# Optimization experiments

Measured on AMD Instinct MI355X. Metric: run time of the kernel, lower is better.

Reference implementation:

```python
import jax, jax.numpy as jnp
import numpy as np
from jax import lax

T = 32768
INPUT = 1024
HIDDEN = 1024
OUTPUT = 1024


def setup_inputs() -> dict:
    key = jax.random.key(0)
    k1, k2, k3, k4, k5 = jax.random.split(key, 5)
    return {
        "x": jax.random.normal(k1, (1, T, INPUT), dtype=jnp.float32),
        "W_i2h": jax.random.normal(k2, (HIDDEN, INPUT + HIDDEN), dtype=jnp.float32) * 0.02,
        "b_i2h": jax.random.normal(k3, (HIDDEN,), dtype=jnp.float32) * 0.02,
        "W_h2o": jax.random.normal(k4, (OUTPUT, HIDDEN), dtype=jnp.float32) * 0.02,
        "b_h2o": jax.random.normal(k5, (OUTPUT,), dtype=jnp.float32) * 0.02,
    }


def reference(x, W_i2h, b_i2h, W_h2o, b_h2o):
    # x: [1, T, input]; original iterates timesteps of x[0] with batch-1 state.
    seq = x[0]  # [T, input]
    h0 = jnp.zeros((1, HIDDEN), dtype=x.dtype)

    # Split i2h weight so we avoid a per-step concat: [hidden, input+hidden]
    W_x = W_i2h[:, :INPUT]   # acts on token
    W_h = W_i2h[:, INPUT:]   # acts on hidden

    def step(h, x_t):
        # h: [1, hidden], x_t: [input]
        h_new = jnp.tanh(x_t[None, :] @ W_x.T + h @ W_h.T + b_i2h)
        return h_new, None

    h_T, _ = lax.scan(step, h0, seq)
    # Original computes h2o every step but returns only the last output.
    output = h_T @ W_h2o.T + b_h2o  # [1, output]
    return output
```

## Files before the change

### kernel.cpp

```cpp
#include <hip/hip_runtime.h>

#define T_STEPS 32768
#define HID 1024
#define NWG 128
#define RPW 8
#define MBS 8
#define PRE_BYTES ((size_t)T_STEPS * HID * 2)
#define HP_BYTES  (2 * HID * MBS * 8)

typedef float vf4 __attribute__((ext_vector_type(4)));
typedef unsigned long long u64;

__device__ __forceinline__ unsigned short f2bf(float f) {
    unsigned u = __float_as_uint(f);
    u = (u + 0x7fffu + ((u >> 16) & 1u)) >> 16;
    return (unsigned short)u;
}
__device__ __forceinline__ float bf2f(unsigned short s) {
    return __uint_as_float(((unsigned)s) << 16);
}

#define BM 64
#define BN 64
#define BK 16
#define LDST 68

__global__ void __launch_bounds__(256) pre_gemm(
    const float* __restrict__ x, const float* __restrict__ Wi,
    const float* __restrict__ b, unsigned short* __restrict__ pre)
{
    __shared__ float As[BK * LDST];
    __shared__ float Bs[BK * LDST];
    const int tid = threadIdx.x;
    const int t0 = blockIdx.x * BM;
    const int j0 = blockIdx.y * BN;
    const int row = tid >> 2;
    const int kq  = tid & 3;
    const int tx  = tid & 15;
    const int ty  = tid >> 4;

    float c[4][4];
#pragma unroll
    for (int i = 0; i < 4; ++i)
#pragma unroll
        for (int j = 0; j < 4; ++j) c[i][j] = 0.f;

    for (int k0 = 0; k0 < 1024; k0 += BK) {
        float4 a4 = *(const float4*)&x[(size_t)(t0 + row) * 1024 + k0 + 4 * kq];
        float4 b4 = *(const float4*)&Wi[(size_t)(j0 + row) * 2048 + k0 + 4 * kq];
        __syncthreads();
        As[(4 * kq + 0) * LDST + row] = a4.x;
        As[(4 * kq + 1) * LDST + row] = a4.y;
        As[(4 * kq + 2) * LDST + row] = a4.z;
        As[(4 * kq + 3) * LDST + row] = a4.w;
        Bs[(4 * kq + 0) * LDST + row] = b4.x;
        Bs[(4 * kq + 1) * LDST + row] = b4.y;
        Bs[(4 * kq + 2) * LDST + row] = b4.z;
        Bs[(4 * kq + 3) * LDST + row] = b4.w;
        __syncthreads();
#pragma unroll
        for (int kk = 0; kk < BK; ++kk) {
            float4 av = *(const float4*)&As[kk * LDST + 4 * ty];
            float4 bv = *(const float4*)&Bs[kk * LDST + 4 * tx];
            c[0][0] = fmaf(av.x, bv.x, c[0][0]); c[0][1] = fmaf(av.x, bv.y, c[0][1]);
            c[0][2] = fmaf(av.x, bv.z, c[0][2]); c[0][3] = fmaf(av.x, bv.w, c[0][3]);
            c[1][0] = fmaf(av.y, bv.x, c[1][0]); c[1][1] = fmaf(av.y, bv.y, c[1][1]);
            c[1][2] = fmaf(av.y, bv.z, c[1][2]); c[1][3] = fmaf(av.y, bv.w, c[1][3]);
            c[2][0] = fmaf(av.z, bv.x, c[2][0]); c[2][1] = fmaf(av.z, bv.y, c[2][1]);
            c[2][2] = fmaf(av.z, bv.z, c[2][2]); c[2][3] = fmaf(av.z, bv.w, c[2][3]);
            c[3][0] = fmaf(av.w, bv.x, c[3][0]); c[3][1] = fmaf(av.w, bv.y, c[3][1]);
            c[3][2] = fmaf(av.w, bv.z, c[3][2]); c[3][3] = fmaf(av.w, bv.w, c[3][3]);
        }
    }

    float4 bias = *(const float4*)&b[j0 + 4 * tx];
#pragma unroll
    for (int i = 0; i < 4; ++i) {
        int r = t0 + 4 * ty + i;
        ushort4 u;
        u.x = f2bf(c[i][0] + bias.x);
        u.y = f2bf(c[i][1] + bias.y);
        u.z = f2bf(c[i][2] + bias.z);
        u.w = f2bf(c[i][3] + bias.w);
        *(ushort4*)&pre[(size_t)r * 1024 + j0 + 4 * tx] = u;
    }
}

__device__ __forceinline__ vf4 ldg4_pin(const float* p) {
    vf4 r;
    asm volatile("global_load_dwordx4 %0, %1, off\n\ts_waitcnt vmcnt(0)"
                 : "=v"(r) : "v"(p) : "memory");
    return r;
}
__device__ __forceinline__ u64 pack_hv(float v, unsigned t) {
    return ((u64)t << 32) | (u64)__float_as_uint(v);
}
__device__ __forceinline__ float fast_tanh(float x) {
    float a = fabsf(x);
    float e = __expf(a + a);
    float r = 1.f - 2.f * __builtin_amdgcn_rcpf(e + 1.f);
    return copysignf(r, x);
}

__global__ void __launch_bounds__(512, 2) rnn_rec(
    const unsigned short* __restrict__ pre,
    const float* __restrict__ Wi,
    const float* __restrict__ Wo,
    const float* __restrict__ bo,
    float* __restrict__ out,
    u64* hp)
{
    const int tid = threadIdx.x;
    const int w   = tid >> 6;
    const int l   = tid & 63;
    const int r   = blockIdx.x * RPW + w;

    __shared__ __align__(16) float hl[2][HID];
    __shared__ int s_abort;
    if (tid == 0) s_abort = 0;

    vf4 wv0, wv1, wv2, wv3;
    {
        const float* wp = Wi + (size_t)r * 2048 + 1024 + 4 * l;
        wv0 = ldg4_pin(wp + 0);
        wv1 = ldg4_pin(wp + 256);
        wv2 = ldg4_pin(wp + 512);
        wv3 = ldg4_pin(wp + 768);
    }
    __syncthreads();

    int budget = 8000000;
    const int e0 = 2 * tid, e1 = 2 * tid + 1;

    for (int t = 1; t <= T_STEPS; ++t) {
        const int par = (t - 1) & 1;

        float prev = 0.f;
        if (l == 0) prev = bf2f(pre[(size_t)(t - 1) * HID + r]);

        {
            const u64* s0 = hp + (size_t)par * (HID * MBS) + (size_t)e0 * MBS;
            const u64* s1 = hp + (size_t)par * (HID * MBS) + (size_t)e1 * MBS;
            const unsigned tg = (unsigned)(t - 1);
            u64 q0, q1;
            for (;;) {
                q0 = __hip_atomic_load(s0, __ATOMIC_RELAXED, __HIP_MEMORY_SCOPE_AGENT);
                q1 = __hip_atomic_load(s1, __ATOMIC_RELAXED, __HIP_MEMORY_SCOPE_AGENT);
                if (((unsigned)(q0 >> 32) == tg) & ((unsigned)(q1 >> 32) == tg)) break;
                if (--budget < 0) { s_abort = 1; break; }
            }
            float2 v;
            v.x = __uint_as_float((unsigned)q0);
            v.y = __uint_as_float((unsigned)q1);
            *(float2*)&hl[par][e0] = v;
        }
        __syncthreads();
        if (s_abort) return;

        const float* hb = hl[par];
        vf4 a0 = *(const vf4*)&hb[4 * l + 0];
        vf4 a1 = *(const vf4*)&hb[4 * l + 256];
        vf4 a2 = *(const vf4*)&hb[4 * l + 512];
        vf4 a3 = *(const vf4*)&hb[4 * l + 768];
        float acc0 = 0.f, acc1 = 0.f;
        acc0 = fmaf(wv0.x, a0.x, acc0); acc0 = fmaf(wv0.y, a0.y, acc0);
        acc0 = fmaf(wv0.z, a0.z, acc0); acc0 = fmaf(wv0.w, a0.w, acc0);
        acc1 = fmaf(wv1.x, a1.x, acc1); acc1 = fmaf(wv1.y, a1.y, acc1);
        acc1 = fmaf(wv1.z, a1.z, acc1); acc1 = fmaf(wv1.w, a1.w, acc1);
        acc0 = fmaf(wv2.x, a2.x, acc0); acc0 = fmaf(wv2.y, a2.y, acc0);
        acc0 = fmaf(wv2.z, a2.z, acc0); acc0 = fmaf(wv2.w, a2.w, acc0);
        acc1 = fmaf(wv3.x, a3.x, acc1); acc1 = fmaf(wv3.y, a3.y, acc1);
        acc1 = fmaf(wv3.z, a3.z, acc1); acc1 = fmaf(wv3.w, a3.w, acc1);
        float s = acc0 + acc1;
        s += __shfl_xor(s, 1);
        s += __shfl_xor(s, 2);
        s += __shfl_xor(s, 4);
        s += __shfl_xor(s, 8);
        s += __shfl_xor(s, 16);
        s += __shfl_xor(s, 32);

        if (l == 0) {
            float h = fast_tanh(prev + s);
            __hip_atomic_store(&hp[(size_t)(t & 1) * (HID * MBS) + (size_t)r * MBS],
                               pack_hv(h, (unsigned)t),
                               __ATOMIC_RELAXED, __HIP_MEMORY_SCOPE_AGENT);
        }
    }

    {
        const int par = T_STEPS & 1;
        const u64* s0 = hp + (size_t)par * (HID * MBS) + (size_t)e0 * MBS;
        const u64* s1 = hp + (size_t)par * (HID * MBS) + (size_t)e1 * MBS;
        const unsigned tg = (unsigned)T_STEPS;
        u64 q0, q1;
        for (;;) {
            q0 = __hip_atomic_load(s0, __ATOMIC_RELAXED, __HIP_MEMORY_SCOPE_AGENT);
            q1 = __hip_atomic_load(s1, __ATOMIC_RELAXED, __HIP_MEMORY_SCOPE_AGENT);
            if (((unsigned)(q0 >> 32) == tg) & ((unsigned)(q1 >> 32) == tg)) break;
            if (--budget < 0) { s_abort = 1; break; }
        }
        float2 v;
        v.x = __uint_as_float((unsigned)q0);
        v.y = __uint_as_float((unsigned)q1);
        *(float2*)&hl[0][e0] = v;
        __syncthreads();
        if (s_abort) return;

        const float* hb = hl[0];
        const float* wo = Wo + (size_t)r * 1024 + 4 * l;
        vf4 a0 = *(const vf4*)&hb[4 * l + 0];
        vf4 a1 = *(const vf4*)&hb[4 * l + 256];
        vf4 a2 = *(const vf4*)&hb[4 * l + 512];
        vf4 a3 = *(const vf4*)&hb[4 * l + 768];
        vf4 w0 = *(const vf4*)&wo[0];
        vf4 w1 = *(const vf4*)&wo[256];
        vf4 w2 = *(const vf4*)&wo[512];
        vf4 w3 = *(const vf4*)&wo[768];
        float acc0 = 0.f, acc1 = 0.f;
        acc0 = fmaf(w0.x, a0.x, acc0); acc0 = fmaf(w0.y, a0.y, acc0);
        acc0 = fmaf(w0.z, a0.z, acc0); acc0 = fmaf(w0.w, a0.w, acc0);
        acc1 = fmaf(w1.x, a1.x, acc1); acc1 = fmaf(w1.y, a1.y, acc1);
        acc1 = fmaf(w1.z, a1.z, acc1); acc1 = fmaf(w1.w, a1.w, acc1);
        acc0 = fmaf(w2.x, a2.x, acc0); acc0 = fmaf(w2.y, a2.y, acc0);
        acc0 = fmaf(w2.z, a2.z, acc0); acc0 = fmaf(w2.w, a2.w, acc0);
        acc1 = fmaf(w3.x, a3.x, acc1); acc1 = fmaf(w3.y, a3.y, acc1);
        acc1 = fmaf(w3.z, a3.z, acc1); acc1 = fmaf(w3.w, a3.w, acc1);
        float s = acc0 + acc1;
        s += __shfl_xor(s, 1);
        s += __shfl_xor(s, 2);
        s += __shfl_xor(s, 4);
        s += __shfl_xor(s, 8);
        s += __shfl_xor(s, 16);
        s += __shfl_xor(s, 32);
        if (l == 0) out[r] = s + bo[r];
    }
}

extern "C" void kernel_launch(void* const* d_in, const int* in_sizes, int n_in,
                              void* d_out, int out_size, void* d_ws, size_t ws_size,
                              hipStream_t stream) {
    const float* x     = (const float*)d_in[0];
    const float* W_i2h = (const float*)d_in[1];
    const float* b_i2h = (const float*)d_in[2];
    const float* W_h2o = (const float*)d_in[3];
    const float* b_h2o = (const float*)d_in[4];
    float* out = (float*)d_out;

    char* base = (char*)d_ws;
    unsigned short* pre = (unsigned short*)base;
    u64* hp = (u64*)(base + PRE_BYTES);

    hipMemsetAsync(hp, 0, HP_BYTES, stream);
    pre_gemm<<<dim3(T_STEPS / BM, HID / BN), 256, 0, stream>>>(x, W_i2h, b_i2h, pre);
    rnn_rec<<<NWG, 512, 0, stream>>>(pre, W_i2h, W_h2o, b_h2o, out, hp);
}
```

Measured before the change: 63.74 ms.

## Pack hidden-state flags densely and poll with one wave using vector loads

The per-step hidden-state exchange buffer drops its 8-slot padding per element, so the tagged values are stored contiguously. Only wave 0 of each workgroup now polls, with eight dwordx4 loads per lane covering 16 elements, and it re-issues only the chunks whose tags are not yet current. It then writes the gathered values into LDS for the other waves. This cuts the number of polling memory requests and the atomic traffic per step. In exchange, neighbouring writers now share cache lines, and the other seven waves sit idle at the barrier while wave 0 polls.

```diff
diff --git a/kernel.cpp b/kernel.cpp
--- a/kernel.cpp
+++ b/kernel.cpp
@@ -4,11 +4,11 @@
 #define HID 1024
 #define NWG 128
 #define RPW 8
-#define MBS 8
 #define PRE_BYTES ((size_t)T_STEPS * HID * 2)
-#define HP_BYTES  (2 * HID * MBS * 8)
+#define HP_BYTES  (2 * HID * 8)
 
 typedef float vf4 __attribute__((ext_vector_type(4)));
+typedef unsigned uv4 __attribute__((ext_vector_type(4)));
 typedef unsigned long long u64;
 
 __device__ __forceinline__ unsigned short f2bf(float f) {
@@ -102,6 +102,56 @@
     return copysignf(r, x);
 }
 
+#define POLL_CHUNK(c, qq)                                                     \
+    if (!(done & (1u << c)))                                                  \
+        asm volatile("global_load_dwordx4 %0, %1, off offset:" #c "6 sc1"     \
+                     : "=v"(qq) : "v"(pp));
+
+__device__ __forceinline__ void poll_wave0(const u64* par_base, unsigned tg,
+                                           float* dstLDS, int l, int& budget,
+                                           int* s_abort)
+{
+    const u64* pp = par_base + (size_t)l * 16;
+    uv4 q0, q1, q2, q3, q4, q5, q6, q7;
+    unsigned done = 0;
+    for (;;) {
+        if (!(done & 0x01u)) asm volatile("global_load_dwordx4 %0, %1, off sc1"            : "=v"(q0) : "v"(pp));
+        if (!(done & 0x02u)) asm volatile("global_load_dwordx4 %0, %1, off offset:16 sc1"  : "=v"(q1) : "v"(pp));
+        if (!(done & 0x04u)) asm volatile("global_load_dwordx4 %0, %1, off offset:32 sc1"  : "=v"(q2) : "v"(pp));
+        if (!(done & 0x08u)) asm volatile("global_load_dwordx4 %0, %1, off offset:48 sc1"  : "=v"(q3) : "v"(pp));
+        if (!(done & 0x10u)) asm volatile("global_load_dwordx4 %0, %1, off offset:64 sc1"  : "=v"(q4) : "v"(pp));
+        if (!(done & 0x20u)) asm volatile("global_load_dwordx4 %0, %1, off offset:80 sc1"  : "=v"(q5) : "v"(pp));
+        if (!(done & 0x40u)) asm volatile("global_load_dwordx4 %0, %1, off offset:96 sc1"  : "=v"(q6) : "v"(pp));
+        if (!(done & 0x80u)) asm volatile("global_load_dwordx4 %0, %1, off offset:112 sc1" : "=v"(q7) : "v"(pp));
+        asm volatile("s_waitcnt vmcnt(0)"
+                     : "+v"(q0), "+v"(q1), "+v"(q2), "+v"(q3),
+                       "+v"(q4), "+v"(q5), "+v"(q6), "+v"(q7));
+        done |= ((q0.y == tg) & (q0.w == tg)) ? 0x01u : 0u;
+        done |= ((q1.y == tg) & (q1.w == tg)) ? 0x02u : 0u;
+        done |= ((q2.y == tg) & (q2.w == tg)) ? 0x04u : 0u;
+        done |= ((q3.y == tg) & (q3.w == tg)) ? 0x08u : 0u;
+        done |= ((q4.y == tg) & (q4.w == tg)) ? 0x10u : 0u;
+        done |= ((q5.y == tg) & (q5.w == tg)) ? 0x20u : 0u;
+        done |= ((q6.y == tg) & (q6.w == tg)) ? 0x40u : 0u;
+        done |= ((q7.y == tg) & (q7.w == tg)) ? 0x80u : 0u;
+        if (done == 0xffu) break;
+        if (--budget < 0) { *s_abort = 1; break; }
+    }
+    float* d = dstLDS + 16 * l;
+    vf4 v0 = (vf4){__uint_as_float(q0.x), __uint_as_float(q0.z),
+                   __uint_as_float(q1.x), __uint_as_float(q1.z)};
+    vf4 v1 = (vf4){__uint_as_float(q2.x), __uint_as_float(q2.z),
+                   __uint_as_float(q3.x), __uint_as_float(q3.z)};
+    vf4 v2 = (vf4){__uint_as_float(q4.x), __uint_as_float(q4.z),
+                   __uint_as_float(q5.x), __uint_as_float(q5.z)};
+    vf4 v3 = (vf4){__uint_as_float(q6.x), __uint_as_float(q6.z),
+                   __uint_as_float(q7.x), __uint_as_float(q7.z)};
+    *(vf4*)&d[0]  = v0;
+    *(vf4*)&d[4]  = v1;
+    *(vf4*)&d[8]  = v2;
+    *(vf4*)&d[12] = v3;
+}
+
 __global__ void __launch_bounds__(512, 2) rnn_rec(
     const unsigned short* __restrict__ pre,
     const float* __restrict__ Wi,
@@ -130,7 +180,6 @@
     __syncthreads();
 
     int budget = 8000000;
-    const int e0 = 2 * tid, e1 = 2 * tid + 1;
 
     for (int t = 1; t <= T_STEPS; ++t) {
         const int par = (t - 1) & 1;
@@ -138,22 +187,9 @@
         float prev = 0.f;
         if (l == 0) prev = bf2f(pre[(size_t)(t - 1) * HID + r]);
 
-        {
-            const u64* s0 = hp + (size_t)par * (HID * MBS) + (size_t)e0 * MBS;
-            const u64* s1 = hp + (size_t)par * (HID * MBS) + (size_t)e1 * MBS;
-            const unsigned tg = (unsigned)(t - 1);
-            u64 q0, q1;
-            for (;;) {
-                q0 = __hip_atomic_load(s0, __ATOMIC_RELAXED, __HIP_MEMORY_SCOPE_AGENT);
-                q1 = __hip_atomic_load(s1, __ATOMIC_RELAXED, __HIP_MEMORY_SCOPE_AGENT);
-                if (((unsigned)(q0 >> 32) == tg) & ((unsigned)(q1 >> 32) == tg)) break;
-                if (--budget < 0) { s_abort = 1; break; }
-            }
-            float2 v;
-            v.x = __uint_as_float((unsigned)q0);
-            v.y = __uint_as_float((unsigned)q1);
-            *(float2*)&hl[par][e0] = v;
-        }
+        if (w == 0)
+            poll_wave0(hp + (size_t)par * HID, (unsigned)(t - 1),
+                       hl[par], l, budget, &s_abort);
         __syncthreads();
         if (s_abort) return;
 
@@ -181,7 +217,7 @@
 
         if (l == 0) {
             float h = fast_tanh(prev + s);
-            __hip_atomic_store(&hp[(size_t)(t & 1) * (HID * MBS) + (size_t)r * MBS],
+            __hip_atomic_store(&hp[(size_t)(t & 1) * HID + r],
                                pack_hv(h, (unsigned)t),
                                __ATOMIC_RELAXED, __HIP_MEMORY_SCOPE_AGENT);
         }
@@ -189,20 +225,9 @@
 
     {
         const int par = T_STEPS & 1;
-        const u64* s0 = hp + (size_t)par * (HID * MBS) + (size_t)e0 * MBS;
-        const u64* s1 = hp + (size_t)par * (HID * MBS) + (size_t)e1 * MBS;
-        const unsigned tg = (unsigned)T_STEPS;
-        u64 q0, q1;
-        for (;;) {
-            q0 = __hip_atomic_load(s0, __ATOMIC_RELAXED, __HIP_MEMORY_SCOPE_AGENT);
-            q1 = __hip_atomic_load(s1, __ATOMIC_RELAXED, __HIP_MEMORY_SCOPE_AGENT);
-            if (((unsigned)(q0 >> 32) == tg) & ((unsigned)(q1 >> 32) == tg)) break;
-            if (--budget < 0) { s_abort = 1; break; }
-        }
-        float2 v;
-        v.x = __uint_as_float((unsigned)q0);
-        v.y = __uint_as_float((unsigned)q1);
-        *(float2*)&hl[0][e0] = v;
+        if (w == 0)
+            poll_wave0(hp + (size_t)par * HID, (unsigned)T_STEPS,
+                       hl[0], l, budget, &s_abort);
         __syncthreads();
         if (s_abort) return;
 
```

New measurement: 62.83 ms. About the same (-1.4%).
